# Performance work log

Hardware: AMD Instinct MI355X
Metric: run time of the kernel (lower is better)

## Reference

```python
import jax, jax.numpy as jnp
import numpy as np

B, C, N = 4, 512, 4096
CH = C // 2  # query/key projection dim


def setup_inputs() -> dict:
    key = jax.random.key(0)
    ks = jax.random.split(key, 10)
    s = 1.0 / np.sqrt(C)
    return {
        "Q": jax.random.normal(ks[0], (B, C, N), dtype=jnp.float32),
        "K": jax.random.normal(ks[1], (B, C, N), dtype=jnp.float32),
        "V": jax.random.normal(ks[2], (B, C, N), dtype=jnp.float32),
        "Wq": jax.random.normal(ks[3], (CH, C), dtype=jnp.float32) * s,
        "bq": jax.random.normal(ks[4], (CH,), dtype=jnp.float32) * s,
        "Wk": jax.random.normal(ks[5], (CH, C), dtype=jnp.float32) * s,
        "bk": jax.random.normal(ks[6], (CH,), dtype=jnp.float32) * s,
        "Wv": jax.random.normal(ks[7], (C, C), dtype=jnp.float32) * s,
        "bv": jax.random.normal(ks[8], (C,), dtype=jnp.float32) * s,
        "gamma": jnp.full((1,), 0.5, dtype=jnp.float32),  # torch inits to 0; nonzero for meaningful math
    }


def reference(Q, K, V, Wq, bq, Wk, bk, Wv, bv, gamma):
    # Conv1d(kernel_size=1) == per-position linear over channels
    q = jnp.einsum("oc,bcn->bon", Wq, Q) + bq[None, :, None]  # [B, C/2, N]
    k = jnp.einsum("oc,bcn->bon", Wk, K) + bk[None, :, None]  # [B, C/2, N]
    v = jnp.einsum("oc,bcn->bon", Wv, V) + bv[None, :, None]  # [B, C, N]
    # energy[b,n,m] = <q[b,:,n], k[b,:,m]>  (no 1/sqrt(d) scaling in original)
    energy = jnp.einsum("bcn,bcm->bnm", q, k)                 # [B, N, N]
    attention = jax.nn.softmax(energy, axis=-1)
    # out[b,c,n] = sum_m v[b,c,m] * attention[b,n,m]
    out = jnp.einsum("bcm,bnm->bcn", v, attention)            # [B, C, N]
    return gamma * out + V
```

## Files before the change

kernel.cpp:

```cpp
#include <hip/hip_runtime.h>
#include <cstdint>
#include <cstddef>

constexpr int B_  = 4;
constexpr int C_  = 512;
constexpr int CH_ = 256;
constexpr int N_  = 4096;
#define LOG2E 1.4426950408889634f

typedef float    f32x4 __attribute__((ext_vector_type(4)));
typedef _Float16 f16x8 __attribute__((ext_vector_type(8)));
typedef _Float16 f16x4 __attribute__((ext_vector_type(4)));

__device__ __forceinline__ f32x4 MFMA16(f16x8 a, f16x8 b, f32x4 c) {
  return __builtin_amdgcn_mfma_f32_16x16x32_f16(a, b, c, 0, 0, 0);
}

typedef const __attribute__((address_space(1))) unsigned int* gas_u32p;
typedef __attribute__((address_space(3))) unsigned int* las_u32p;
__device__ __forceinline__ void async16(const void* g, void* l) {
  __builtin_amdgcn_global_load_lds((gas_u32p)g, (las_u32p)l, 16, 0, 0);
}

__global__ void prep_w_kernel(const float* __restrict__ Wq,
                              const float* __restrict__ Wk,
                              const float* __restrict__ Wv,
                              _Float16* __restrict__ wq,
                              _Float16* __restrict__ wk,
                              _Float16* __restrict__ wv) {
  int i = blockIdx.x * 256 + threadIdx.x;
  if (i < CH_ * C_) {
    wq[i] = (_Float16)(Wq[i] * LOG2E);
    wk[i] = (_Float16)Wk[i];
  }
  if (i < C_ * C_) wv[i] = (_Float16)Wv[i];
}

__global__ __launch_bounds__(512, 4) void proj_kernel(
    const _Float16* __restrict__ wq, const _Float16* __restrict__ wk,
    const _Float16* __restrict__ wv, const float* __restrict__ Q,
    const float* __restrict__ K, const float* __restrict__ V,
    const float* __restrict__ bq, const float* __restrict__ bk,
    const float* __restrict__ bv, _Float16* __restrict__ qT,
    _Float16* __restrict__ kT, _Float16* __restrict__ vT) {
  __shared__ __align__(16) _Float16 lW[2][256 * 32];
  __shared__ __align__(16) _Float16 lX[2][64 * 56];

  const int y = blockIdx.y;
  const _Float16* W;
  const float* X;
  const float* bias;
  _Float16* out;
  int o0 = 0, M, mode;
  float bscale = 1.0f;
  if (y == 0) {
    W = wq; X = Q; bias = bq; out = qT; M = CH_; mode = 0; bscale = LOG2E;
  } else if (y == 1) {
    W = wk; X = K; bias = bk; out = kT; M = CH_; mode = 0;
  } else {
    W = wv; X = V; bias = bv; out = vT; M = C_; mode = 1; o0 = (y - 2) * 256;
  }

  const int tid = threadIdx.x;
  const int lane = tid & 63, wave = tid >> 6;
  const int g = lane >> 4, lm = lane & 15;
  const int b = blockIdx.z;
  const int n0 = blockIdx.x * 64;
  const int wo = (wave >> 1) * 64, wn = (wave & 1) * 32;

  const _Float16* Wb = W + (size_t)o0 * C_;
  const float* Xb = X + (size_t)b * C_ * N_;

  f32x4 acc[8];
#pragma unroll
  for (int i = 0; i < 8; ++i) acc[i] = f32x4{0.f, 0.f, 0.f, 0.f};

  auto stageW = [&](int s, int buf) {
    int c0 = s * 32;
#pragma unroll
    for (int r = 0; r < 2; ++r) {
      int ci = r * 512 + tid;
      int o = ci >> 2, cg = ci & 3;
      async16(Wb + (size_t)o * C_ + c0 + cg * 8,
              (char*)&lW[buf][0] + r * 8192 + wave * 1024);
    }
  };

  const int xc = tid >> 4;
  const int xn4 = (tid & 15) * 4;
  const int xgran = xc >> 3, xcin = xc & 7;
  auto gloadX = [&](int s) {
    return *(const f32x4*)(Xb + (size_t)(s * 32 + xc) * N_ + n0 + xn4);
  };
  auto writeX = [&](int buf, f32x4 v) {
#pragma unroll
    for (int i = 0; i < 4; ++i) {
      int n = xn4 + i;
      int pos = (xgran ^ ((n >> 2) & 3)) * 8 + xcin;
      lX[buf][n * 56 + pos] = (_Float16)v[i];
    }
  };

  f32x4 xg = gloadX(0);
  writeX(0, xg);
  xg = gloadX(1);
  stageW(0, 0);
  __syncthreads();

#pragma unroll
  for (int s = 0; s < 16; ++s) {
    const int cb = s & 1, nb = cb ^ 1;
    if (s < 15) stageW(s + 1, nb);
    f32x4 xgn;
    if (s < 14) xgn = gloadX(s + 2);

    f16x8 wf[4], xf[2];
#pragma unroll
    for (int ot = 0; ot < 4; ++ot)
      wf[ot] = *(const f16x8*)&lW[cb][((wo + ot * 16 + lm) * 4 + g) * 8];
#pragma unroll
    for (int nt = 0; nt < 2; ++nt) {
      int n = wn + nt * 16 + lm;
      int pos = (g ^ ((n >> 2) & 3)) * 8;
      xf[nt] = *(const f16x8*)&lX[cb][n * 56 + pos];
    }

    if (mode == 0) {
#pragma unroll
      for (int nt = 0; nt < 2; ++nt)
#pragma unroll
        for (int ot = 0; ot < 4; ++ot)
          acc[nt * 4 + ot] = MFMA16(xf[nt], wf[ot], acc[nt * 4 + ot]);
    } else {
#pragma unroll
      for (int ot = 0; ot < 4; ++ot)
#pragma unroll
        for (int nt = 0; nt < 2; ++nt)
          acc[ot * 2 + nt] = MFMA16(wf[ot], xf[nt], acc[ot * 2 + nt]);
    }

    if (s < 15) writeX(nb, xg);
    if (s < 14) xg = xgn;
    __syncthreads();
  }

  if (mode == 0) {
#pragma unroll
    for (int nt = 0; nt < 2; ++nt) {
#pragma unroll
      for (int ot = 0; ot < 4; ++ot) {
        int o = wo + ot * 16 + lm;
        float bv_ = bias[o] * bscale;
#pragma unroll
        for (int r = 0; r < 4; ++r) {
          int n = n0 + wn + nt * 16 + g * 4 + r;
          out[((size_t)b * N_ + n) * M + o] =
              (_Float16)(acc[nt * 4 + ot][r] + bv_);
        }
      }
    }
  } else {
#pragma unroll
    for (int ot = 0; ot < 4; ++ot) {
#pragma unroll
      for (int r = 0; r < 4; ++r) {
        int o = o0 + wo + ot * 16 + g * 4 + r;
        float bv_ = bias[o];
#pragma unroll
        for (int nt = 0; nt < 2; ++nt) {
          int n = n0 + wn + nt * 16 + lm;
          out[((size_t)b * M + o) * N_ + n] =
              (_Float16)(acc[ot * 2 + nt][r] + bv_);
        }
      }
    }
  }
}

__global__ __launch_bounds__(512, 2) void attn_kernel(
    const _Float16* __restrict__ qT, const _Float16* __restrict__ kT,
    const _Float16* __restrict__ vT, float* __restrict__ Op0,
    _Float16* __restrict__ Op0h, _Float16* __restrict__ Op1,
    float* __restrict__ mbuf, float* __restrict__ lbuf, int op0f16) {
  __shared__ __align__(16) _Float16 kstage[2 * 8192];
  __shared__ __align__(16) _Float16 P_t[128 * 72];
  __shared__ float al_st[128];
  __shared__ int bumped[8];

  const int tid = threadIdx.x;
  const int lane = tid & 63, wave = tid >> 6;
  const int g = lane >> 4, lm = lane & 15;

  const int bx = blockIdx.x;
  const int xcd = bx & 7;
  const int b = xcd >> 1, h = xcd & 1;
  const int n0 = (bx >> 3) * 128;
  const int mbase = h * 2048;
  const int c0w = wave * 64;

  f32x4 O[4][8];
#pragma unroll
  for (int i = 0; i < 4; ++i)
#pragma unroll
    for (int j = 0; j < 8; ++j) O[i][j] = f32x4{0.f, 0.f, 0.f, 0.f};
  f32x4 Ol = f32x4{0.f, 0.f, 0.f, 0.f};

  const _Float16* qTb = qT + ((size_t)b * N_ + n0) * CH_;
  f16x8 qf[8];
#pragma unroll
  for (int p = 0; p < 2; ++p) {
#pragma unroll
    for (int r = 0; r < 4; ++r) {
      int sidx = r * 512 + tid;
      int rl = sidx >> 5, cgs = sidx & 31;
      async16(qTb + (size_t)(p * 64 + rl) * CH_ + ((cgs ^ (rl & 7)) * 8),
              (char*)kstage + r * 8192 + wave * 1024);
    }
    __syncthreads();
    if ((wave >> 2) == p) {
      int rl = (wave & 3) * 16 + lm;
#pragma unroll
      for (int ks = 0; ks < 8; ++ks)
        qf[ks] =
            *(const f16x8*)&kstage[rl * 256 + (((ks * 4 + g) ^ (rl & 7)) * 8)];
    }
    __syncthreads();
  }

  const _Float16* kTb = kT + ((size_t)b * N_ + mbase) * CH_;
  auto stage_k = [&](int it) {
    int m0 = it * 32;
    char* dst0 = (char*)kstage + (it & 1) * 16384;
#pragma unroll
    for (int r = 0; r < 2; ++r) {
      int sidx = r * 512 + tid;
      int key = sidx >> 5, cgs = sidx & 31;
      async16(kTb + (size_t)(m0 + key) * CH_ + ((cgs ^ (key & 7)) * 8),
              dst0 + r * 8192 + wave * 1024);
    }
  };
  stage_k(0);

  const _Float16* vTb = vT + (size_t)b * C_ * N_ + mbase;
  const _Float16* vbase[4];
#pragma unroll
  for (int ct = 0; ct < 4; ++ct)
    vbase[ct] = vTb + (size_t)(c0w + ct * 16 + lm) * N_ + g * 8;
  f16x8 vf[4], vfn[4];
#pragma unroll
  for (int ct = 0; ct < 4; ++ct) vf[ct] = *(const f16x8*)vbase[ct];

  float m_run = -1e30f;
  f16x8 ones;
#pragma unroll
  for (int i = 0; i < 8; ++i) ones[i] = (_Float16)1.0f;

#pragma unroll 1
  for (int it = 0; it < 64; ++it) {
    __syncthreads();
    if (it < 63) stage_k(it + 1);

    const _Float16* kb = kstage + (it & 1) * 8192;
    f32x4 s0 = f32x4{0.f, 0.f, 0.f, 0.f};
    f32x4 s1 = f32x4{0.f, 0.f, 0.f, 0.f};
    const int key0 = lm, key1 = 16 + lm;
#pragma unroll
    for (int ks = 0; ks < 8; ++ks) {
      f16x8 kf0 =
          *(const f16x8*)&kb[key0 * 256 + (((ks * 4 + g) ^ (key0 & 7)) * 8)];
      f16x8 kf1 =
          *(const f16x8*)&kb[key1 * 256 + (((ks * 4 + g) ^ (key1 & 7)) * 8)];
      s0 = MFMA16(kf0, qf[ks], s0);
      s1 = MFMA16(kf1, qf[ks], s1);
    }

    float mx = fmaxf(fmaxf(fmaxf(s0[0], s0[1]), fmaxf(s0[2], s0[3])),
                     fmaxf(fmaxf(s1[0], s1[1]), fmaxf(s1[2], s1[3])));
    mx = fmaxf(mx, __shfl_xor(mx, 16));
    mx = fmaxf(mx, __shfl_xor(mx, 32));
    bool need = (mx > m_run + 8.0f);
    float mnew = need ? mx : m_run;
    float alpha = need ? exp2f(m_run - mnew) : 1.0f;
    m_run = mnew;
    f16x4 pa, pb;
#pragma unroll
    for (int r = 0; r < 4; ++r) {
      pa[r] = (_Float16)exp2f(s0[r] - mnew);
      pb[r] = (_Float16)exp2f(s1[r] - mnew);
    }
    const int prow = wave * 16 + lm;
    *(f16x4*)&P_t[prow * 72 + g * 4] = pa;
    *(f16x4*)&P_t[prow * 72 + 16 + g * 4] = pb;
    if (g == 0) al_st[prow] = alpha;
    unsigned long long bal = __ballot(need);
    if (lane == 0) bumped[wave] = (bal != 0ull) ? 1 : 0;
    __syncthreads();

    if (it < 63) {
      int mo = (it + 1) * 32;
#pragma unroll
      for (int ct = 0; ct < 4; ++ct)
        vfn[ct] = *(const f16x8*)(vbase[ct] + mo);
    }

#pragma unroll
    for (int nt = 0; nt < 8; ++nt) {
      if (__builtin_amdgcn_readfirstlane(bumped[nt])) {
        float a = al_st[nt * 16 + lm];
#pragma unroll
        for (int ct = 0; ct < 4; ++ct) {
          O[ct][nt][0] *= a; O[ct][nt][1] *= a;
          O[ct][nt][2] *= a; O[ct][nt][3] *= a;
        }
      }
    }
    if (__builtin_amdgcn_readfirstlane(bumped[wave])) {
      float a = al_st[wave * 16 + lm];
      Ol[0] *= a; Ol[1] *= a; Ol[2] *= a; Ol[3] *= a;
    }

#pragma unroll
    for (int nt = 0; nt < 8; ++nt) {
      f16x8 pf = *(const f16x8*)&P_t[(nt * 16 + lm) * 72 + g * 8];
#pragma unroll
      for (int ct = 0; ct < 4; ++ct) O[ct][nt] = MFMA16(vf[ct], pf, O[ct][nt]);
    }
    {
      f16x8 pfo = *(const f16x8*)&P_t[(wave * 16 + lm) * 72 + g * 8];
      Ol = MFMA16(ones, pfo, Ol);
    }
    if (it < 63) {
#pragma unroll
      for (int ct = 0; ct < 4; ++ct) vf[ct] = vfn[ct];
    }
  }

  const size_t hb = (size_t)(b * 2 + h) * N_ + n0;
  if (g == 0) mbuf[hb + wave * 16 + lm] = m_run;
  if (lane < 16) lbuf[hb + wave * 16 + lane] = Ol[0];

  if (h == 0 && !op0f16) {
    float* ob = Op0 + (size_t)b * C_ * N_;
#pragma unroll
    for (int nt = 0; nt < 8; ++nt) {
      int n_g = n0 + nt * 16 + lm;
#pragma unroll
      for (int ct = 0; ct < 4; ++ct) {
        int cb = c0w + ct * 16 + g * 4;
#pragma unroll
        for (int r = 0; r < 4; ++r)
          ob[(size_t)(cb + r) * N_ + n_g] = O[ct][nt][r];
      }
    }
  } else {
    _Float16* ob = (h == 0 ? Op0h : Op1) + (size_t)b * C_ * N_;
#pragma unroll
    for (int nt = 0; nt < 8; ++nt) {
      int n_g = n0 + nt * 16 + lm;
#pragma unroll
      for (int ct = 0; ct < 4; ++ct) {
        int cb = c0w + ct * 16 + g * 4;
#pragma unroll
        for (int r = 0; r < 4; ++r)
          ob[(size_t)(cb + r) * N_ + n_g] = (_Float16)O[ct][nt][r];
      }
    }
  }
}

__global__ __launch_bounds__(256) void combine_kernel(
    float* __restrict__ out, const _Float16* __restrict__ Op0h,
    const _Float16* __restrict__ Op1, const float* __restrict__ mbuf,
    const float* __restrict__ lbuf, const float* __restrict__ Vin,
    const float* __restrict__ gptr, int op0f16) {
  const int b = blockIdx.y;
  const int tid = threadIdx.x;
  const int n = blockIdx.x * 64 + (tid & 15) * 4;
  const int cg = tid >> 4;
  const float gamma = gptr[0];

  float s0[4], s1[4];
#pragma unroll
  for (int j = 0; j < 4; ++j) {
    float m0 = mbuf[(size_t)(b * 2 + 0) * N_ + n + j];
    float m1 = mbuf[(size_t)(b * 2 + 1) * N_ + n + j];
    float mx = fmaxf(m0, m1);
    float a0 = exp2f(m0 - mx), a1 = exp2f(m1 - mx);
    float l = a0 * lbuf[(size_t)(b * 2 + 0) * N_ + n + j] +
              a1 * lbuf[(size_t)(b * 2 + 1) * N_ + n + j];
    float inv = gamma / l;
    s0[j] = a0 * inv;
    s1[j] = a1 * inv;
  }

  const _Float16* O0b = Op0h + (size_t)b * C_ * N_;
  const _Float16* O1b = Op1 + (size_t)b * C_ * N_;
  if (op0f16) {
    for (int c = cg * 32; c < cg * 32 + 32; ++c) {
      size_t idx = ((size_t)b * C_ + c) * N_ + n;
      f16x4 p0 = *(const f16x4*)(O0b + (size_t)c * N_ + n);
      f16x4 p1 = *(const f16x4*)(O1b + (size_t)c * N_ + n);
      f32x4 V = *(const f32x4*)(Vin + idx);
      f32x4 r;
#pragma unroll
      for (int j = 0; j < 4; ++j)
        r[j] = (float)p0[j] * s0[j] + (float)p1[j] * s1[j] + V[j];
      *(f32x4*)(out + idx) = r;
    }
  } else {
    for (int c = cg * 32; c < cg * 32 + 32; ++c) {
      size_t idx = ((size_t)b * C_ + c) * N_ + n;
      f32x4 p0 = *(const f32x4*)(out + idx);
      f16x4 p1 = *(const f16x4*)(O1b + (size_t)c * N_ + n);
      f32x4 V = *(const f32x4*)(Vin + idx);
      f32x4 r;
#pragma unroll
      for (int j = 0; j < 4; ++j)
        r[j] = p0[j] * s0[j] + (float)p1[j] * s1[j] + V[j];
      *(f32x4*)(out + idx) = r;
    }
  }
}

extern "C" void kernel_launch(void* const* d_in, const int* in_sizes, int n_in,
                              void* d_out, int out_size, void* d_ws, size_t ws_size,
                              hipStream_t stream) {
  const float* Q  = (const float*)d_in[0];
  const float* K  = (const float*)d_in[1];
  const float* V  = (const float*)d_in[2];
  const float* Wq = (const float*)d_in[3];
  const float* bq = (const float*)d_in[4];
  const float* Wk = (const float*)d_in[5];
  const float* bk = (const float*)d_in[6];
  const float* Wv = (const float*)d_in[7];
  const float* bv = (const float*)d_in[8];
  const float* gm = (const float*)d_in[9];
  float* out = (float*)d_out;

  char* p = (char*)d_ws;
  _Float16* wq = (_Float16*)p; p += (size_t)CH_ * C_ * 2;
  _Float16* wk = (_Float16*)p; p += (size_t)CH_ * C_ * 2;
  _Float16* wv = (_Float16*)p; p += (size_t)C_ * C_ * 2;
  _Float16* qT = (_Float16*)p; p += (size_t)B_ * N_ * CH_ * 2;
  _Float16* kT = (_Float16*)p; p += (size_t)B_ * N_ * CH_ * 2;
  _Float16* vT = (_Float16*)p; p += (size_t)B_ * C_ * N_ * 2;
  _Float16* Op1 = (_Float16*)p; p += (size_t)B_ * C_ * N_ * 2;
  float* mbuf = (float*)p; p += (size_t)B_ * 2 * N_ * 4;
  float* lbuf = (float*)p; p += (size_t)B_ * 2 * N_ * 4;
  _Float16* Op0h = (_Float16*)p;
  size_t need = (size_t)(p - (char*)d_ws) + (size_t)B_ * C_ * N_ * 2;
  int op0f16 = (ws_size >= need) ? 1 : 0;

  prep_w_kernel<<<(C_ * C_) / 256, 256, 0, stream>>>(Wq, Wk, Wv, wq, wk, wv);

  proj_kernel<<<dim3(N_ / 64, 4, B_), 512, 0, stream>>>(
      wq, wk, wv, Q, K, V, bq, bk, bv, qT, kT, vT);

  attn_kernel<<<256, 512, 0, stream>>>(qT, kT, vT, out, Op0h, Op1, mbuf, lbuf,
                                       op0f16);

  combine_kernel<<<dim3(N_ / 64, B_), 256, 0, stream>>>(out, Op0h, Op1, mbuf,
                                                        lbuf, V, gm, op0f16);
}
```

Baseline: 358.9 us.

## Pre-transpose inputs to fp16 and use async-LDS projection kernel

Measured after the change: 366.5 us. 2.1% more time.

```diff
diff --git a/kernel.cpp b/kernel.cpp
--- a/kernel.cpp
+++ b/kernel.cpp
@@ -34,6 +34,167 @@
     wk[i] = (_Float16)Wk[i];
   }
   if (i < C_ * C_) wv[i] = (_Float16)Wv[i];
+}
+
+__global__ __launch_bounds__(256) void prep_x_kernel(
+    const float* __restrict__ Q, const float* __restrict__ K,
+    const float* __restrict__ V, _Float16* __restrict__ XTq,
+    _Float16* __restrict__ XTk, _Float16* __restrict__ XTv) {
+  __shared__ _Float16 t[64][68];
+
+  const int z = blockIdx.z;
+  const int b = z / 3, ip = z - 3 * b;
+  const float* X = (ip == 0) ? Q : (ip == 1) ? K : V;
+  _Float16* O = (ip == 0) ? XTq : (ip == 1) ? XTk : XTv;
+
+  const int c0 = blockIdx.y * 64, n0 = blockIdx.x * 64;
+  const int tid = threadIdx.x;
+  const int tr = tid >> 4, tc4 = (tid & 15) * 4;
+
+  const float* Xb = X + (size_t)b * C_ * N_;
+#pragma unroll
+  for (int it = 0; it < 4; ++it) {
+    int c = it * 16 + tr;
+    f32x4 v = *(const f32x4*)(Xb + (size_t)(c0 + c) * N_ + n0 + tc4);
+#pragma unroll
+    for (int j = 0; j < 4; ++j) t[tc4 + j][c] = (_Float16)v[j];
+  }
+  __syncthreads();
+  _Float16* Ob = O + (size_t)b * N_ * C_;
+#pragma unroll
+  for (int it = 0; it < 4; ++it) {
+    int n = it * 16 + tr;
+    f16x4 w = *(const f16x4*)&t[n][tc4];
+    *(f16x4*)(Ob + (size_t)(n0 + n) * C_ + c0 + tc4) = w;
+  }
+}
+
+__global__ __launch_bounds__(512, 4) void proj2_kernel(
+    const _Float16* __restrict__ wq, const _Float16* __restrict__ wk,
+    const _Float16* __restrict__ wv, const _Float16* __restrict__ XTq,
+    const _Float16* __restrict__ XTk, const _Float16* __restrict__ XTv,
+    const float* __restrict__ bq, const float* __restrict__ bk,
+    const float* __restrict__ bv, _Float16* __restrict__ qT,
+    _Float16* __restrict__ kT, _Float16* __restrict__ vT) {
+  __shared__ __align__(16) _Float16 lW[2][256 * 32];
+  __shared__ __align__(16) _Float16 lX[2][64 * 32];
+
+  const int y = blockIdx.y;
+  const _Float16* W;
+  const _Float16* XT;
+  const float* bias;
+  _Float16* out;
+  int o0 = 0, M, mode;
+  float bscale = 1.0f;
+  if (y == 0) {
+    W = wq; XT = XTq; bias = bq; out = qT; M = CH_; mode = 0; bscale = LOG2E;
+  } else if (y == 1) {
+    W = wk; XT = XTk; bias = bk; out = kT; M = CH_; mode = 0;
+  } else {
+    W = wv; XT = XTv; bias = bv; out = vT; M = C_; mode = 1; o0 = (y - 2) * 256;
+  }
+
+  const int tid = threadIdx.x;
+  const int lane = tid & 63, wave = tid >> 6;
+  const int g = lane >> 4, lm = lane & 15;
+  const int b = blockIdx.z;
+  const int n0 = blockIdx.x * 64;
+  const int wo = (wave >> 1) * 64, wn = (wave & 1) * 32;
+
+  const _Float16* Wb = W + (size_t)o0 * C_;
+  const _Float16* XTb = XT + (size_t)b * N_ * C_;
+
+  f32x4 acc[8];
+#pragma unroll
+  for (int i = 0; i < 8; ++i) acc[i] = f32x4{0.f, 0.f, 0.f, 0.f};
+
+  auto stageW = [&](int s, int buf) {
+    int c0 = s * 32;
+#pragma unroll
+    for (int r = 0; r < 2; ++r) {
+      int ci = r * 512 + tid;
+      int o = ci >> 2, cg = ci & 3;
+      async16(Wb + (size_t)o * C_ + c0 + cg * 8,
+              (char*)&lW[buf][0] + r * 8192 + wave * 1024);
+    }
+  };
+  auto stageX = [&](int s, int buf) {
+    if (tid < 256) {
+      int rl = tid >> 2, cgs = tid & 3;
+      async16(XTb + (size_t)(n0 + rl) * C_ + s * 32 + ((cgs ^ (rl & 3)) * 8),
+              (char*)&lX[buf][0] + wave * 1024);
+    }
+  };
+
+  stageW(0, 0);
+  stageX(0, 0);
+  __syncthreads();
+
+#pragma unroll
+  for (int s = 0; s < 16; ++s) {
+    const int cb = s & 1, nb = cb ^ 1;
+    if (s < 15) {
+      stageW(s + 1, nb);
+      stageX(s + 1, nb);
+    }
+
+    f16x8 wf[4], xf[2];
+#pragma unroll
+    for (int ot = 0; ot < 4; ++ot)
+      wf[ot] = *(const f16x8*)&lW[cb][((wo + ot * 16 + lm) * 4 + g) * 8];
+#pragma unroll
+    for (int nt = 0; nt < 2; ++nt) {
+      int nl = wn + nt * 16 + lm;
+      xf[nt] = *(const f16x8*)&lX[cb][nl * 32 + ((g ^ (nl & 3)) * 8)];
+    }
+
+    if (mode == 0) {
+#pragma unroll
+      for (int nt = 0; nt < 2; ++nt)
+#pragma unroll
+        for (int ot = 0; ot < 4; ++ot)
+          acc[nt * 4 + ot] = MFMA16(xf[nt], wf[ot], acc[nt * 4 + ot]);
+    } else {
+#pragma unroll
+      for (int ot = 0; ot < 4; ++ot)
+#pragma unroll
+        for (int nt = 0; nt < 2; ++nt)
+          acc[ot * 2 + nt] = MFMA16(wf[ot], xf[nt], acc[ot * 2 + nt]);
+    }
+    __syncthreads();
+  }
+
+  if (mode == 0) {
+#pragma unroll
+    for (int nt = 0; nt < 2; ++nt) {
+#pragma unroll
+      for (int ot = 0; ot < 4; ++ot) {
+        int o = wo + ot * 16 + lm;
+        float bv_ = bias[o] * bscale;
+#pragma unroll
+        for (int r = 0; r < 4; ++r) {
+          int n = n0 + wn + nt * 16 + g * 4 + r;
+          out[((size_t)b * N_ + n) * M + o] =
+              (_Float16)(acc[nt * 4 + ot][r] + bv_);
+        }
+      }
+    }
+  } else {
+#pragma unroll
+    for (int ot = 0; ot < 4; ++ot) {
+#pragma unroll
+      for (int r = 0; r < 4; ++r) {
+        int o = o0 + wo + ot * 16 + g * 4 + r;
+        float bv_ = bias[o];
+#pragma unroll
+        for (int nt = 0; nt < 2; ++nt) {
+          int n = n0 + wn + nt * 16 + lm;
+          out[((size_t)b * M + o) * N_ + n] =
+              (_Float16)(acc[ot * 2 + nt][r] + bv_);
+        }
+      }
+    }
+  }
 }
 
 __global__ __launch_bounds__(512, 4) void proj_kernel(
@@ -444,21 +605,40 @@
   _Float16* qT = (_Float16*)p; p += (size_t)B_ * N_ * CH_ * 2;
   _Float16* kT = (_Float16*)p; p += (size_t)B_ * N_ * CH_ * 2;
   _Float16* vT = (_Float16*)p; p += (size_t)B_ * C_ * N_ * 2;
-  _Float16* Op1 = (_Float16*)p; p += (size_t)B_ * C_ * N_ * 2;
   float* mbuf = (float*)p; p += (size_t)B_ * 2 * N_ * 4;
   float* lbuf = (float*)p; p += (size_t)B_ * 2 * N_ * 4;
-  _Float16* Op0h = (_Float16*)p;
-  size_t need = (size_t)(p - (char*)d_ws) + (size_t)B_ * C_ * N_ * 2;
-  int op0f16 = (ws_size >= need) ? 1 : 0;
+
+  const size_t xtsz = (size_t)B_ * N_ * C_ * 2;
+  size_t base = (size_t)(p - (char*)d_ws);
 
   prep_w_kernel<<<(C_ * C_) / 256, 256, 0, stream>>>(Wq, Wk, Wv, wq, wk, wv);
 
-  proj_kernel<<<dim3(N_ / 64, 4, B_), 512, 0, stream>>>(
-      wq, wk, wv, Q, K, V, bq, bk, bv, qT, kT, vT);
-
-  attn_kernel<<<256, 512, 0, stream>>>(qT, kT, vT, out, Op0h, Op1, mbuf, lbuf,
-                                       op0f16);
-
-  combine_kernel<<<dim3(N_ / 64, B_), 256, 0, stream>>>(out, Op0h, Op1, mbuf,
-                                                        lbuf, V, gm, op0f16);
-}
+  if (ws_size >= base + 3 * xtsz) {
+    _Float16* XTq = (_Float16*)p;
+    _Float16* XTk = (_Float16*)(p + xtsz);
+    _Float16* XTv = (_Float16*)(p + 2 * xtsz);
+    _Float16* Op1 = XTq;
+    _Float16* Op0h = XTk;
+
+    prep_x_kernel<<<dim3(N_ / 64, C_ / 64, B_ * 3), 256, 0, stream>>>(
+        Q, K, V, XTq, XTk, XTv);
+    proj2_kernel<<<dim3(N_ / 64, 4, B_), 512, 0, stream>>>(
+        wq, wk, wv, XTq, XTk, XTv, bq, bk, bv, qT, kT, vT);
+    attn_kernel<<<256, 512, 0, stream>>>(qT, kT, vT, out, Op0h, Op1, mbuf,
+                                         lbuf, 1);
+    combine_kernel<<<dim3(N_ / 64, B_), 256, 0, stream>>>(out, Op0h, Op1, mbuf,
+                                                          lbuf, V, gm, 1);
+  } else {
+    _Float16* Op1 = (_Float16*)p; p += (size_t)B_ * C_ * N_ * 2;
+    _Float16* Op0h = (_Float16*)p;
+    size_t need = (size_t)(p - (char*)d_ws) + (size_t)B_ * C_ * N_ * 2;
+    int op0f16 = (ws_size >= need) ? 1 : 0;
+
+    proj_kernel<<<dim3(N_ / 64, 4, B_), 512, 0, stream>>>(
+        wq, wk, wv, Q, K, V, bq, bk, bv, qT, kT, vT);
+    attn_kernel<<<256, 512, 0, stream>>>(qT, kT, vT, out, Op0h, Op1, mbuf,
+                                         lbuf, op0f16);
+    combine_kernel<<<dim3(N_ / 64, B_), 256, 0, stream>>>(out, Op0h, Op1, mbuf,
+                                                          lbuf, V, gm, op0f16);
+  }
+}
```
